# Performance work log

Measured on AMD Instinct MI355X. Metric: run time of the kernel, lower is better.

The kernel has to match this reference:

```python
import jax, jax.numpy as jnp
import numpy as np

N = 100000

def _gcn_layer(x, W, b, src, dst, norm):
    # dense transform then sparse normalized aggregation (scatter-add)
    h = x @ W                                  # [N, out]
    msg = h[src] * norm[:, None]               # [E+N, out]
    agg = jax.ops.segment_sum(msg, dst, num_segments=N)
    return agg + b


def setup_inputs() -> dict:
    key = jax.random.key(0)
    ks = jax.random.split(key, 12)
    num_features, hidden, num_classes = 128, 128, 32
    E = 3200000
    x = jax.random.normal(ks[0], (N, num_features), dtype=jnp.float32)
    edge_index = jax.random.randint(ks[1], (2, E), 0, N, dtype=jnp.int64)

    def glorot(k, fan_in, fan_out):
        s = (6.0 / (fan_in + fan_out)) ** 0.5
        return jax.random.uniform(k, (fan_in, fan_out), jnp.float32, -s, s)

    return {
        "x": x,
        "edge_index": edge_index,
        "W1": glorot(ks[2], num_features, hidden), "b1": jnp.zeros((hidden,), jnp.float32),
        "W2": glorot(ks[3], hidden, hidden),       "b2": jnp.zeros((hidden,), jnp.float32),
        "W3": glorot(ks[4], hidden, hidden),       "b3": jnp.zeros((hidden,), jnp.float32),
        "W4": glorot(ks[5], hidden, num_classes),  "b4": jnp.zeros((num_classes,), jnp.float32),
    }


def reference(x, edge_index, W1, b1, W2, b2, W3, b3, W4, b4):
    # GCNConv semantics: add self-loops, symmetric degree normalization
    loop = jnp.arange(N, dtype=edge_index.dtype)
    src = jnp.concatenate([edge_index[0], loop])   # [E+N]
    dst = jnp.concatenate([edge_index[1], loop])   # [E+N]
    deg = jax.ops.segment_sum(jnp.ones_like(dst, dtype=x.dtype), dst, num_segments=N)
    dinv = jnp.where(deg > 0, deg ** -0.5, 0.0)
    norm = dinv[src] * dinv[dst]                   # [E+N]

    h = _gcn_layer(x, W1, b1, src, dst, norm)
    h = jax.nn.relu(h)                              # dropout: eval mode -> identity
    h = _gcn_layer(h, W2, b2, src, dst, norm)
    h = jax.nn.relu(h)
    h = _gcn_layer(h, W3, b3, src, dst, norm)
    h = jax.nn.relu(h)
    h = _gcn_layer(h, W4, b4, src, dst, norm)
    return jax.nn.log_softmax(h, axis=1)
```

## Files before the change

kernel.cpp:

```cpp
#include <hip/hip_runtime.h>
#include <hip/hip_bf16.h>
#include <math.h>

#define NNODES 100000
#define NBMAX 512
#define CH 8192

typedef __hip_bfloat16 bf16;
typedef __attribute__((ext_vector_type(8))) short short8;
typedef __attribute__((ext_vector_type(4))) float f32x4;
typedef __attribute__((ext_vector_type(2))) float f32x2;

__device__ inline unsigned pack_bf16x2(float a, float b) {
    __hip_bfloat162 p;
    p.x = __float2bfloat16(a);
    p.y = __float2bfloat16(b);
    return *(unsigned*)&p;
}

__device__ inline float2 unpack_bf16x2(unsigned u) {
    __hip_bfloat162 p = *(__hip_bfloat162*)&u;
    return make_float2(__bfloat162float(p.x), __bfloat162float(p.y));
}

__device__ inline unsigned char f32_to_fp8(float v) {
    int p = __builtin_amdgcn_cvt_pk_fp8_f32(v, v, 0, false);
    return (unsigned char)(p & 0xff);
}

__global__ __launch_bounds__(256) void bucket_hist(const int* __restrict__ dst,
                                                   int* __restrict__ bcount, int E, int nb) {
    __shared__ int hist[NBMAX];
    int t = threadIdx.x;
    for (int i = t; i < NBMAX; i += 256) hist[i] = 0;
    __syncthreads();
    int e0 = blockIdx.x * CH;
#pragma unroll
    for (int k = 0; k < 32; ++k) {
        int e = e0 + t + k * 256;
        if (e < E) atomicAdd(&hist[dst[e] >> 8], 1);
    }
    __syncthreads();
    for (int i = t; i < nb; i += 256)
        if (hist[i]) atomicAdd(&bcount[i], hist[i]);
}

__global__ __launch_bounds__(512) void bucket_scan(const int* __restrict__ bcount,
                                                   int* __restrict__ boff,
                                                   int* __restrict__ bcursor,
                                                   int* __restrict__ off, int nb, int n) {
    __shared__ int wsum[8];
    int t = threadIdx.x;
    int v = (t < nb) ? bcount[t] : 0;
    int lane = t & 63, wv = t >> 6;
    int incl = v;
#pragma unroll
    for (int d = 1; d < 64; d <<= 1) {
        int x = __shfl_up(incl, d, 64);
        if (lane >= d) incl += x;
    }
    if (lane == 63) wsum[wv] = incl;
    __syncthreads();
    int wo = 0;
    for (int k = 0; k < wv; ++k) wo += wsum[k];
    int excl = wo + incl - v;
    if (t <= nb) {
        boff[t] = excl;
        if (t < nb) bcursor[t] = excl;
    }
    if (t == nb) off[n] = excl;
}

__global__ __launch_bounds__(256) void partition(const int* __restrict__ src,
                                                 const int* __restrict__ dst,
                                                 int* __restrict__ bcursor,
                                                 int2* __restrict__ part, int E, int nb) {
    __shared__ int hist[NBMAX];
    __shared__ int lstart[NBMAX];
    __shared__ int gbase[NBMAX];
    __shared__ int cursor[NBMAX];
    __shared__ int2 sorted[CH];
    int t = threadIdx.x;
    int e0 = blockIdx.x * CH;
    for (int i = t; i < NBMAX; i += 256) hist[i] = 0;
    __syncthreads();
    int mys[32], myd[32];
#pragma unroll
    for (int k = 0; k < 32; ++k) {
        int e = e0 + t + k * 256;
        int s = 0, d = -1;
        if (e < E) { s = src[e]; d = dst[e]; }
        mys[k] = s; myd[k] = d;
        if (d >= 0) atomicAdd(&hist[d >> 8], 1);
    }
    __syncthreads();
    if (t < 64) {
        int base = t * 8;
        int tmp[8];
        int sum = 0;
#pragma unroll
        for (int j = 0; j < 8; ++j) { tmp[j] = hist[base + j]; sum += tmp[j]; }
        int incl = sum;
#pragma unroll
        for (int d = 1; d < 64; d <<= 1) {
            int x = __shfl_up(incl, d, 64);
            if (t >= d) incl += x;
        }
        int excl = incl - sum;
#pragma unroll
        for (int j = 0; j < 8; ++j) {
            lstart[base + j] = excl;
            cursor[base + j] = excl;
            excl += tmp[j];
        }
    }
    __syncthreads();
    for (int i = t; i < nb; i += 256) {
        int c = hist[i];
        gbase[i] = c ? atomicAdd(&bcursor[i], c) : 0;
    }
    __syncthreads();
#pragma unroll
    for (int k = 0; k < 32; ++k) {
        int d = myd[k];
        if (d >= 0) {
            int lpos = atomicAdd(&cursor[d >> 8], 1);
            sorted[lpos] = make_int2(mys[k], d);
        }
    }
    __syncthreads();
    int cnt = min(CH, E - e0);
    for (int i = t; i < cnt; i += 256) {
        int2 rec = sorted[i];
        int b = rec.y >> 8;
        part[gbase[b] + (i - lstart[b])] = rec;
    }
}

__global__ __launch_bounds__(256) void nodes_fill(const int2* __restrict__ part,
                                                  const int* __restrict__ boff,
                                                  float* __restrict__ dinv,
                                                  int* __restrict__ off,
                                                  int* __restrict__ edges, int n) {
    __shared__ int ndeg[256];
    __shared__ int ws2[4];
    __shared__ int offl[256];
    int b = blockIdx.x;
    int t = threadIdx.x;
    ndeg[t] = 0;
    __syncthreads();
    int r0 = boff[b], r1 = boff[b + 1];
    for (int i = r0 + t; i < r1; i += 256)
        atomicAdd(&ndeg[part[i].y & 255], 1);
    __syncthreads();
    int deg = ndeg[t];
    int node = b * 256 + t;
    int lane = t & 63, wv = t >> 6;
    int incl = deg;
#pragma unroll
    for (int d = 1; d < 64; d <<= 1) {
        int x = __shfl_up(incl, d, 64);
        if (lane >= d) incl += x;
    }
    if (lane == 63) ws2[wv] = incl;
    __syncthreads();
    int wo = 0;
    for (int k = 0; k < wv; ++k) wo += ws2[k];
    int node_off = r0 + wo + incl - deg;
    if (node < n) {
        off[node] = node_off;
        dinv[node] = rsqrtf((float)(deg + 1));
    }
    offl[t] = node_off;
    ndeg[t] = 0;
    __syncthreads();
    for (int i = r0 + t; i < r1; i += 256) {
        int2 rec = part[i];
        int dloc = rec.y & 255;
        int lpos = atomicAdd(&ndeg[dloc], 1);
        edges[offl[dloc] + lpos] = rec.x;
    }
}

__global__ void prep_w(const float* __restrict__ W, bf16* __restrict__ WT, int K, int Nout) {
    int idx = blockIdx.x * blockDim.x + threadIdx.x;
    if (idx >= K * Nout) return;
    int nn = idx / K;
    int kk = idx - nn * K;
    WT[idx] = __float2bfloat16(W[kk * Nout + nn]);
}

#define WSTRIDE 136

__global__ __launch_bounds__(256) void gemm128_f32A(const float* __restrict__ A,
                                                    const bf16* __restrict__ WT,
                                                    const float* __restrict__ dinv,
                                                    unsigned char* __restrict__ C, int n) {
    __shared__ bf16 wl[128 * WSTRIDE];
    int t = threadIdx.x;
#pragma unroll
    for (int l = 0; l < 8; ++l) {
        int chunk = t + l * 256;
        int row = chunk >> 4, ch = chunk & 15;
        *(uint4*)&wl[row * WSTRIDE + ch * 8] = *(const uint4*)&WT[row * 128 + ch * 8];
    }
    __syncthreads();
    int wave = t >> 6, lane = t & 63;
    int m = lane & 15, q = lane >> 4;
    int row_base = blockIdx.x * 128 + wave * 32;
    int r0 = min(row_base + m, n - 1);
    int r1 = min(row_base + 16 + m, n - 1);

    f32x4 acc[2][8];
#pragma unroll
    for (int g = 0; g < 2; ++g)
#pragma unroll
        for (int c = 0; c < 8; ++c) acc[g][c] = (f32x4)(0.f);

#pragma unroll
    for (int kt = 0; kt < 4; ++kt) {
        short8 af[2];
#pragma unroll
        for (int g = 0; g < 2; ++g) {
            const float* ap = &A[(size_t)(g ? r1 : r0) * 128 + kt * 32 + q * 8];
            float4 f0 = *(const float4*)ap;
            float4 f1 = *(const float4*)(ap + 4);
            union { uint4 u; short8 s; } cv;
            cv.u.x = pack_bf16x2(f0.x, f0.y);
            cv.u.y = pack_bf16x2(f0.z, f0.w);
            cv.u.z = pack_bf16x2(f1.x, f1.y);
            cv.u.w = pack_bf16x2(f1.z, f1.w);
            af[g] = cv.s;
        }
#pragma unroll
        for (int c = 0; c < 8; ++c) {
            short8 bf = *(const short8*)&wl[(c * 16 + m) * WSTRIDE + kt * 32 + q * 8];
            acc[0][c] = __builtin_amdgcn_mfma_f32_16x16x32_bf16(af[0], bf, acc[0][c], 0, 0, 0);
            acc[1][c] = __builtin_amdgcn_mfma_f32_16x16x32_bf16(af[1], bf, acc[1][c], 0, 0, 0);
        }
    }
    float dv[2][4];
#pragma unroll
    for (int g = 0; g < 2; ++g)
#pragma unroll
        for (int r = 0; r < 4; ++r) {
            int row = row_base + g * 16 + q * 4 + r;
            dv[g][r] = (row < n) ? dinv[row] : 0.f;
        }
#pragma unroll
    for (int g = 0; g < 2; ++g)
#pragma unroll
        for (int c = 0; c < 8; ++c)
#pragma unroll
            for (int r = 0; r < 4; ++r) {
                int row = row_base + g * 16 + q * 4 + r;
                if (row < n) C[(size_t)row * 128 + c * 16 + m] = f32_to_fp8(acc[g][c][r] * dv[g][r]);
            }
}

__global__ __launch_bounds__(256) void gemm128_bf16A(const bf16* __restrict__ A,
                                                     const bf16* __restrict__ WT,
                                                     const float* __restrict__ dinv,
                                                     unsigned char* __restrict__ C, int n) {
    __shared__ bf16 wl[128 * WSTRIDE];
    int t = threadIdx.x;
#pragma unroll
    for (int l = 0; l < 8; ++l) {
        int chunk = t + l * 256;
        int row = chunk >> 4, ch = chunk & 15;
        *(uint4*)&wl[row * WSTRIDE + ch * 8] = *(const uint4*)&WT[row * 128 + ch * 8];
    }
    __syncthreads();
    int wave = t >> 6, lane = t & 63;
    int m = lane & 15, q = lane >> 4;
    int row_base = blockIdx.x * 128 + wave * 32;
    int r0 = min(row_base + m, n - 1);
    int r1 = min(row_base + 16 + m, n - 1);

    f32x4 acc[2][8];
#pragma unroll
    for (int g = 0; g < 2; ++g)
#pragma unroll
        for (int c = 0; c < 8; ++c) acc[g][c] = (f32x4)(0.f);

#pragma unroll
    for (int kt = 0; kt < 4; ++kt) {
        short8 a0 = *(const short8*)&A[(size_t)r0 * 128 + kt * 32 + q * 8];
        short8 a1 = *(const short8*)&A[(size_t)r1 * 128 + kt * 32 + q * 8];
#pragma unroll
        for (int c = 0; c < 8; ++c) {
            short8 bf = *(const short8*)&wl[(c * 16 + m) * WSTRIDE + kt * 32 + q * 8];
            acc[0][c] = __builtin_amdgcn_mfma_f32_16x16x32_bf16(a0, bf, acc[0][c], 0, 0, 0);
            acc[1][c] = __builtin_amdgcn_mfma_f32_16x16x32_bf16(a1, bf, acc[1][c], 0, 0, 0);
        }
    }
    float dv[2][4];
#pragma unroll
    for (int g = 0; g < 2; ++g)
#pragma unroll
        for (int r = 0; r < 4; ++r) {
            int row = row_base + g * 16 + q * 4 + r;
            dv[g][r] = (row < n) ? dinv[row] : 0.f;
        }
#pragma unroll
    for (int g = 0; g < 2; ++g)
#pragma unroll
        for (int c = 0; c < 8; ++c)
#pragma unroll
            for (int r = 0; r < 4; ++r) {
                int row = row_base + g * 16 + q * 4 + r;
                if (row < n) C[(size_t)row * 128 + c * 16 + m] = f32_to_fp8(acc[g][c][r] * dv[g][r]);
            }
}

__global__ __launch_bounds__(256) void gemm32_bf16A(const bf16* __restrict__ A,
                                                    const bf16* __restrict__ WT,
                                                    const float* __restrict__ dinv,
                                                    bf16* __restrict__ C, int n) {
    int wave = threadIdx.x >> 6;
    int lane = threadIdx.x & 63;
    int m = lane & 15;
    int q = lane >> 4;
    int row_base = blockIdx.x * 64 + wave * 16;
    int arow = min(row_base + m, n - 1);

    f32x4 acc[2];
    acc[0] = (f32x4)(0.f);
    acc[1] = (f32x4)(0.f);

#pragma unroll
    for (int kt = 0; kt < 4; ++kt) {
        short8 af = *(const short8*)&A[(size_t)arow * 128 + kt * 32 + q * 8];
#pragma unroll
        for (int c = 0; c < 2; ++c) {
            short8 bf = *(const short8*)&WT[(size_t)(c * 16 + m) * 128 + kt * 32 + q * 8];
            acc[c] = __builtin_amdgcn_mfma_f32_16x16x32_bf16(af, bf, acc[c], 0, 0, 0);
        }
    }
    float dv[4];
#pragma unroll
    for (int r = 0; r < 4; ++r) {
        int row = row_base + q * 4 + r;
        dv[r] = (row < n) ? dinv[row] : 0.f;
    }
#pragma unroll
    for (int c = 0; c < 2; ++c)
#pragma unroll
        for (int r = 0; r < 4; ++r) {
            int row = row_base + q * 4 + r;
            if (row < n) C[(size_t)row * 32 + c * 16 + m] = __float2bfloat16(acc[c][r] * dv[r]);
        }
}

__global__ __launch_bounds__(256) void agg128(const unsigned char* __restrict__ h,
                                              const int* __restrict__ off,
                                              const int* __restrict__ edges,
                                              const float* __restrict__ dinv,
                                              const float* __restrict__ bias,
                                              bf16* __restrict__ out, int n) {
    int wid = (blockIdx.x * blockDim.x + threadIdx.x) >> 6;
    if (wid >= n) return;
    int lane = threadIdx.x & 63;
    int g = lane >> 4;
    int d = lane & 15;
    const char* hb = (const char*)h;
    unsigned doff = (unsigned)(d << 3);

    f32x2 A0 = {0.f, 0.f}, A1 = {0.f, 0.f}, A2 = {0.f, 0.f}, A3 = {0.f, 0.f};
    {
        uint2 su = *(const uint2*)(hb + (((unsigned)wid << 7) | doff));
        if (g) { su.x = 0u; su.y = 0u; }
        A0 += __builtin_amdgcn_cvt_pk_f32_fp8((int)su.x, false);
        A1 += __builtin_amdgcn_cvt_pk_f32_fp8((int)su.x, true);
        A2 += __builtin_amdgcn_cvt_pk_f32_fp8((int)su.y, false);
        A3 += __builtin_amdgcn_cvt_pk_f32_fp8((int)su.y, true);
    }

    int i0 = off[wid], i1 = off[wid + 1];
    int i = i0;
    int id[8];
    if (i + 32 <= i1) {
#pragma unroll
        for (int j = 0; j < 8; ++j) id[j] = edges[i + j * 4 + g];
    }
    while (i + 32 <= i1) {
        uint2 uu[8];
#pragma unroll
        for (int j = 0; j < 8; ++j)
            uu[j] = *(const uint2*)(hb + (((unsigned)id[j] << 7) | doff));
        int inext = i + 32;
        if (inext + 32 <= i1) {
#pragma unroll
            for (int j = 0; j < 8; ++j) id[j] = edges[inext + j * 4 + g];
        }
#pragma unroll
        for (int j = 0; j < 8; ++j) {
            A0 += __builtin_amdgcn_cvt_pk_f32_fp8((int)uu[j].x, false);
            A1 += __builtin_amdgcn_cvt_pk_f32_fp8((int)uu[j].x, true);
            A2 += __builtin_amdgcn_cvt_pk_f32_fp8((int)uu[j].y, false);
            A3 += __builtin_amdgcn_cvt_pk_f32_fp8((int)uu[j].y, true);
        }
        i = inext;
    }
    if (i < i1) {
        int nj = (i1 - i + 3) >> 2;
        uint2 uu[8];
#pragma unroll
        for (int j = 0; j < 8; ++j) {
            if (j < nj) {
                int e = i + j * 4 + g;
                int s = edges[e];
                if (e >= i1) s = n;
                uu[j] = *(const uint2*)(hb + (((unsigned)s << 7) | doff));
            }
        }
#pragma unroll
        for (int j = 0; j < 8; ++j) {
            if (j < nj) {
                A0 += __builtin_amdgcn_cvt_pk_f32_fp8((int)uu[j].x, false);
                A1 += __builtin_amdgcn_cvt_pk_f32_fp8((int)uu[j].x, true);
                A2 += __builtin_amdgcn_cvt_pk_f32_fp8((int)uu[j].y, false);
                A3 += __builtin_amdgcn_cvt_pk_f32_fp8((int)uu[j].y, true);
            }
        }
    }
    float r0 = A0[0], r1 = A0[1], r2 = A1[0], r3 = A1[1];
    float r4 = A2[0], r5 = A2[1], r6 = A3[0], r7 = A3[1];
    r0 += __shfl_xor(r0, 16); r1 += __shfl_xor(r1, 16);
    r2 += __shfl_xor(r2, 16); r3 += __shfl_xor(r3, 16);
    r4 += __shfl_xor(r4, 16); r5 += __shfl_xor(r5, 16);
    r6 += __shfl_xor(r6, 16); r7 += __shfl_xor(r7, 16);
    r0 += __shfl_xor(r0, 32); r1 += __shfl_xor(r1, 32);
    r2 += __shfl_xor(r2, 32); r3 += __shfl_xor(r3, 32);
    r4 += __shfl_xor(r4, 32); r5 += __shfl_xor(r5, 32);
    r6 += __shfl_xor(r6, 32); r7 += __shfl_xor(r7, 32);
    float pa = (g & 1) ? r2 : r0;
    float pb = (g & 1) ? r3 : r1;
    float qa = (g & 1) ? r6 : r4;
    float qb = (g & 1) ? r7 : r5;
    pa = (g & 2) ? qa : pa;
    pb = (g & 2) ? qb : pb;

    float dl = dinv[wid];
    int od = d * 4 + g;
    float2 bv = *(const float2*)&bias[od * 2];
    float a0 = fmaxf(pa * dl + bv.x, 0.f);
    float a1 = fmaxf(pb * dl + bv.y, 0.f);
    ((unsigned*)out)[(size_t)wid * 64 + od] = pack_bf16x2(a0, a1);
}

__global__ __launch_bounds__(256) void agg32_lsm(const bf16* __restrict__ h,
                                                 const int* __restrict__ off,
                                                 const int* __restrict__ edges,
                                                 const float* __restrict__ dinv,
                                                 const float* __restrict__ bias,
                                                 float* __restrict__ out, int n) {
    int idx = blockIdx.x * blockDim.x + threadIdx.x;
    int node = idx >> 5;
    if (node >= n) return;
    int lane5 = idx & 31;
    int sub = lane5 & 15;
    int pr = lane5 >> 4;
    const unsigned* h4 = (const unsigned*)h;

    unsigned su = pr ? 0u : h4[(size_t)node * 16 + sub];
    float2 sf = unpack_bf16x2(su);
    f32x2 acc = {sf.x, sf.y};

    int i0 = off[node], i1 = off[node + 1];
    int i = i0;
    for (; i + 16 <= i1; i += 16) {
        unsigned uu[8];
#pragma unroll
        for (int j = 0; j < 8; ++j) {
            int s = edges[i + j * 2 + pr];
            uu[j] = h4[(size_t)s * 16 + sub];
        }
#pragma unroll
        for (int j = 0; j < 8; ++j) {
            float2 f = unpack_bf16x2(uu[j]);
            acc[0] += f.x; acc[1] += f.y;
        }
    }
    for (; i + 2 <= i1; i += 2) {
        int s = edges[i + pr];
        float2 f = unpack_bf16x2(h4[(size_t)s * 16 + sub]);
        acc[0] += f.x; acc[1] += f.y;
    }
    if (i < i1) {
        unsigned u = pr ? 0u : h4[(size_t)edges[i] * 16 + sub];
        float2 f = unpack_bf16x2(u);
        acc[0] += f.x; acc[1] += f.y;
    }
    float s0 = acc[0] + __shfl_xor(acc[0], 16);
    float s1 = acc[1] + __shfl_xor(acc[1], 16);

    float dl = dinv[node];
    float2 bv = *(const float2*)&bias[sub * 2];
    float a0 = s0 * dl + bv.x;
    float a1 = s1 * dl + bv.y;
    float m = fmaxf(a0, a1);
    for (int d = 8; d; d >>= 1) m = fmaxf(m, __shfl_xor(m, d));
    float e = expf(a0 - m) + expf(a1 - m);
    for (int d = 8; d; d >>= 1) e += __shfl_xor(e, d);
    float lse = m + logf(e);
    if (pr == 0)
        *(float2*)&out[(size_t)node * 32 + sub * 2] = make_float2(a0 - lse, a1 - lse);
}

extern "C" void kernel_launch(void* const* d_in, const int* in_sizes, int n_in,
                              void* d_out, int out_size, void* d_ws, size_t ws_size,
                              hipStream_t stream) {
    const float* x  = (const float*)d_in[0];
    const int*   ei = (const int*)d_in[1];
    const float* W1 = (const float*)d_in[2];
    const float* b1 = (const float*)d_in[3];
    const float* W2 = (const float*)d_in[4];
    const float* b2 = (const float*)d_in[5];
    const float* W3 = (const float*)d_in[6];
    const float* b3 = (const float*)d_in[7];
    const float* W4 = (const float*)d_in[8];
    const float* b4 = (const float*)d_in[9];
    float* out = (float*)d_out;

    const int N = NNODES;
    const int E = in_sizes[1] / 2;
    const int nb = (N + 255) / 256;

    char* ws = (char*)d_ws;
    size_t o = 0;
    auto alloc = [&](size_t bytes) -> void* {
        void* p = ws + o;
        o += (bytes + 255) & ~(size_t)255;
        return p;
    };
    int*   bcount  = (int*)alloc((size_t)NBMAX * 4);
    int*   boff    = (int*)alloc((size_t)(NBMAX + 1) * 4);
    int*   bcursor = (int*)alloc((size_t)NBMAX * 4);
    int*   off     = (int*)alloc((size_t)(N + 1) * 4);
    float* dinv    = (float*)alloc((size_t)N * 4);
    int2*  part    = (int2*)alloc((size_t)E * 8);
    int*   edges   = (int*)alloc((size_t)(E + 64) * 4);
    bf16*  wt1     = (bf16*)alloc((size_t)128 * 128 * 2);
    bf16*  wt2     = (bf16*)alloc((size_t)128 * 128 * 2);
    bf16*  wt3     = (bf16*)alloc((size_t)128 * 128 * 2);
    bf16*  wt4     = (bf16*)alloc((size_t)32 * 128 * 2);
    unsigned char* hbuf = (unsigned char*)alloc((size_t)(N + 1) * 128);
    bf16*  gbuf    = (bf16*)part;

    const int* srcv = ei;
    const int* dstv = ei + E;

    hipMemsetAsync(bcount, 0, (size_t)NBMAX * 4, stream);
    hipMemsetAsync(hbuf + (size_t)N * 128, 0, 128, stream);

    int pblocks = (E + CH - 1) / CH;
    bucket_hist<<<pblocks, 256, 0, stream>>>(dstv, bcount, E, nb);
    bucket_scan<<<1, 512, 0, stream>>>(bcount, boff, bcursor, off, nb, N);
    partition<<<pblocks, 256, 0, stream>>>(srcv, dstv, bcursor, part, E, nb);
    nodes_fill<<<nb, 256, 0, stream>>>(part, boff, dinv, off, edges, N);

    prep_w<<<64, 256, 0, stream>>>(W1, wt1, 128, 128);
    prep_w<<<64, 256, 0, stream>>>(W2, wt2, 128, 128);
    prep_w<<<64, 256, 0, stream>>>(W3, wt3, 128, 128);
    prep_w<<<16, 256, 0, stream>>>(W4, wt4, 128, 32);

    int gemm128_blocks = (N + 127) / 128;
    int gemm32_blocks = (N + 63) / 64;
    int agg128_blocks = (N + 3) / 4;
    int agg32_blocks = (N * 32 + 255) / 256;

    gemm128_f32A<<<gemm128_blocks, 256, 0, stream>>>(x, wt1, dinv, hbuf, N);
    agg128<<<agg128_blocks, 256, 0, stream>>>(hbuf, off, edges, dinv, b1, gbuf, N);
    gemm128_bf16A<<<gemm128_blocks, 256, 0, stream>>>(gbuf, wt2, dinv, hbuf, N);
    agg128<<<agg128_blocks, 256, 0, stream>>>(hbuf, off, edges, dinv, b2, gbuf, N);
    gemm128_bf16A<<<gemm128_blocks, 256, 0, stream>>>(gbuf, wt3, dinv, hbuf, N);
    agg128<<<agg128_blocks, 256, 0, stream>>>(hbuf, off, edges, dinv, b3, gbuf, N);
    gemm32_bf16A<<<gemm32_blocks, 256, 0, stream>>>(gbuf, wt4, dinv, (bf16*)hbuf, N);
    agg32_lsm<<<agg32_blocks, 256, 0, stream>>>((const bf16*)hbuf, off, edges, dinv, b4, out, N);
}
```

Baseline: 499.2 us.

## Merge setup launches and widen gather batches in aggregation kernels

Folds the four weight-transpose launches and the memsets into a single prep kernel, and fuses the bucket histogram with its scan using a last-block ticket counter. This removes several small launches and memset calls. The 128-wide aggregation now loads 16 indices at a time and gathers without cross-iteration prefetch, and the 32-wide aggregation with log-softmax is restructured so each lane handles 8 bytes per edge over 4 edge groups. The 32-wide path now writes a zero padding row for tail loads. The trade-offs are higher register pressure and a last-block scan that relies on atomics and fences.

```diff
diff --git a/kernel.cpp b/kernel.cpp
--- a/kernel.cpp
+++ b/kernel.cpp
@@ -28,9 +28,41 @@
     return (unsigned char)(p & 0xff);
 }
 
-__global__ __launch_bounds__(256) void bucket_hist(const int* __restrict__ dst,
-                                                   int* __restrict__ bcount, int E, int nb) {
+__global__ __launch_bounds__(256) void prep_w_all(const float* __restrict__ W1, bf16* __restrict__ wt1,
+                                                  const float* __restrict__ W2, bf16* __restrict__ wt2,
+                                                  const float* __restrict__ W3, bf16* __restrict__ wt3,
+                                                  const float* __restrict__ W4, bf16* __restrict__ wt4,
+                                                  int* __restrict__ bcount, int* __restrict__ done,
+                                                  unsigned* __restrict__ zrow) {
+    int b = blockIdx.x, t = threadIdx.x;
+    if (b == 0) {
+        for (int i = t; i < NBMAX; i += 256) bcount[i] = 0;
+        if (t == 0) *done = 0;
+        if (t < 32) zrow[t] = 0u;
+    }
+    const float* W; bf16* WT; int Nout, idx0;
+    if (b < 64)       { W = W1; WT = wt1; Nout = 128; idx0 = b * 256; }
+    else if (b < 128) { W = W2; WT = wt2; Nout = 128; idx0 = (b - 64) * 256; }
+    else if (b < 192) { W = W3; WT = wt3; Nout = 128; idx0 = (b - 128) * 256; }
+    else              { W = W4; WT = wt4; Nout = 32;  idx0 = (b - 192) * 256; }
+    int idx = idx0 + t;
+    if (idx < 128 * Nout) {
+        int nn = idx >> 7;
+        int kk = idx & 127;
+        WT[idx] = __float2bfloat16(W[kk * Nout + nn]);
+    }
+}
+
+__global__ __launch_bounds__(256) void bucket_hist_scan(const int* __restrict__ dst,
+                                                        int* __restrict__ bcount,
+                                                        int* __restrict__ boff,
+                                                        int* __restrict__ bcursor,
+                                                        int* __restrict__ off,
+                                                        int* __restrict__ done,
+                                                        int E, int nb, int n, int nblocks) {
     __shared__ int hist[NBMAX];
+    __shared__ int ticket_s;
+    __shared__ int wsum[4];
     int t = threadIdx.x;
     for (int i = t; i < NBMAX; i += 256) hist[i] = 0;
     __syncthreads();
@@ -43,32 +75,31 @@
     __syncthreads();
     for (int i = t; i < nb; i += 256)
         if (hist[i]) atomicAdd(&bcount[i], hist[i]);
-}
-
-__global__ __launch_bounds__(512) void bucket_scan(const int* __restrict__ bcount,
-                                                   int* __restrict__ boff,
-                                                   int* __restrict__ bcursor,
-                                                   int* __restrict__ off, int nb, int n) {
-    __shared__ int wsum[8];
-    int t = threadIdx.x;
-    int v = (t < nb) ? bcount[t] : 0;
+    __threadfence();
+    __syncthreads();
+    if (t == 0) ticket_s = atomicAdd(done, 1);
+    __syncthreads();
+    if (ticket_s != nblocks - 1) return;
+    __threadfence();
+    int i0 = t * 2, i1v = t * 2 + 1;
+    int a  = (i0  < nb) ? atomicAdd(&bcount[i0], 0) : 0;
+    int bb = (i1v < nb) ? atomicAdd(&bcount[i1v], 0) : 0;
+    int v = a + bb;
     int lane = t & 63, wv = t >> 6;
     int incl = v;
 #pragma unroll
-    for (int d = 1; d < 64; d <<= 1) {
-        int x = __shfl_up(incl, d, 64);
-        if (lane >= d) incl += x;
+    for (int dd = 1; dd < 64; dd <<= 1) {
+        int x = __shfl_up(incl, dd, 64);
+        if (lane >= dd) incl += x;
     }
     if (lane == 63) wsum[wv] = incl;
     __syncthreads();
     int wo = 0;
     for (int k = 0; k < wv; ++k) wo += wsum[k];
     int excl = wo + incl - v;
-    if (t <= nb) {
-        boff[t] = excl;
-        if (t < nb) bcursor[t] = excl;
-    }
-    if (t == nb) off[n] = excl;
+    if (i0 <= nb)  { boff[i0]  = excl;     if (i0  < nb) bcursor[i0]  = excl; }
+    if (i1v <= nb) { boff[i1v] = excl + a; if (i1v < nb) bcursor[i1v] = excl + a; }
+    if (t == 255) off[n] = excl + v;
 }
 
 __global__ __launch_bounds__(256) void partition(const int* __restrict__ src,
@@ -182,14 +213,6 @@
     }
 }
 
-__global__ void prep_w(const float* __restrict__ W, bf16* __restrict__ WT, int K, int Nout) {
-    int idx = blockIdx.x * blockDim.x + threadIdx.x;
-    if (idx >= K * Nout) return;
-    int nn = idx / K;
-    int kk = idx - nn * K;
-    WT[idx] = __float2bfloat16(W[kk * Nout + nn]);
-}
-
 #define WSTRIDE 136
 
 __global__ __launch_bounds__(256) void gemm128_f32A(const float* __restrict__ A,
@@ -317,6 +340,8 @@
                                                     const bf16* __restrict__ WT,
                                                     const float* __restrict__ dinv,
                                                     bf16* __restrict__ C, int n) {
+    if (blockIdx.x == 0 && threadIdx.x < 32)
+        C[(size_t)n * 32 + threadIdx.x] = __float2bfloat16(0.f);
     int wave = threadIdx.x >> 6;
     int lane = threadIdx.x & 63;
     int m = lane & 15;
@@ -378,44 +403,42 @@
 
     int i0 = off[wid], i1 = off[wid + 1];
     int i = i0;
-    int id[8];
-    if (i + 32 <= i1) {
-#pragma unroll
-        for (int j = 0; j < 8; ++j) id[j] = edges[i + j * 4 + g];
-    }
-    while (i + 32 <= i1) {
-        uint2 uu[8];
-#pragma unroll
-        for (int j = 0; j < 8; ++j)
-            uu[j] = *(const uint2*)(hb + (((unsigned)id[j] << 7) | doff));
-        int inext = i + 32;
-        if (inext + 32 <= i1) {
-#pragma unroll
-            for (int j = 0; j < 8; ++j) id[j] = edges[inext + j * 4 + g];
-        }
-#pragma unroll
-        for (int j = 0; j < 8; ++j) {
+    while (i1 - i > 64) {
+        int id2[16];
+#pragma unroll
+        for (int j = 0; j < 16; ++j) id2[j] = edges[i + j * 4 + g];
+        uint2 uu[16];
+#pragma unroll
+        for (int j = 0; j < 16; ++j)
+            uu[j] = *(const uint2*)(hb + (((unsigned)id2[j] << 7) | doff));
+#pragma unroll
+        for (int j = 0; j < 16; ++j) {
             A0 += __builtin_amdgcn_cvt_pk_f32_fp8((int)uu[j].x, false);
             A1 += __builtin_amdgcn_cvt_pk_f32_fp8((int)uu[j].x, true);
             A2 += __builtin_amdgcn_cvt_pk_f32_fp8((int)uu[j].y, false);
             A3 += __builtin_amdgcn_cvt_pk_f32_fp8((int)uu[j].y, true);
         }
-        i = inext;
-    }
-    if (i < i1) {
-        int nj = (i1 - i + 3) >> 2;
-        uint2 uu[8];
-#pragma unroll
-        for (int j = 0; j < 8; ++j) {
+        i += 64;
+    }
+    {
+        int rem = i1 - i;
+        int nj = (rem + 3) >> 2;
+        int id2[16];
+        uint2 uu[16];
+#pragma unroll
+        for (int j = 0; j < 16; ++j) {
             if (j < nj) {
                 int e = i + j * 4 + g;
                 int s = edges[e];
                 if (e >= i1) s = n;
-                uu[j] = *(const uint2*)(hb + (((unsigned)s << 7) | doff));
+                id2[j] = s;
             }
         }
 #pragma unroll
-        for (int j = 0; j < 8; ++j) {
+        for (int j = 0; j < 16; ++j)
+            if (j < nj) uu[j] = *(const uint2*)(hb + (((unsigned)id2[j] << 7) | doff));
+#pragma unroll
+        for (int j = 0; j < 16; ++j) {
             if (j < nj) {
                 A0 += __builtin_amdgcn_cvt_pk_f32_fp8((int)uu[j].x, false);
                 A1 += __builtin_amdgcn_cvt_pk_f32_fp8((int)uu[j].x, true);
@@ -459,53 +482,80 @@
     int node = idx >> 5;
     if (node >= n) return;
     int lane5 = idx & 31;
-    int sub = lane5 & 15;
-    int pr = lane5 >> 4;
-    const unsigned* h4 = (const unsigned*)h;
-
-    unsigned su = pr ? 0u : h4[(size_t)node * 16 + sub];
-    float2 sf = unpack_bf16x2(su);
-    f32x2 acc = {sf.x, sf.y};
-
+    int g = lane5 >> 3;
+    int d = lane5 & 7;
+    const char* hb = (const char*)h;
+    unsigned doff = (unsigned)(d << 3);
+
+    f32x2 acc0 = {0.f, 0.f}, acc1 = {0.f, 0.f};
+    {
+        uint2 su = *(const uint2*)(hb + (((unsigned)node << 6) | doff));
+        if (g) { su.x = 0u; su.y = 0u; }
+        float2 f0 = unpack_bf16x2(su.x), f1 = unpack_bf16x2(su.y);
+        acc0[0] += f0.x; acc0[1] += f0.y; acc1[0] += f1.x; acc1[1] += f1.y;
+    }
     int i0 = off[node], i1 = off[node + 1];
     int i = i0;
-    for (; i + 16 <= i1; i += 16) {
-        unsigned uu[8];
-#pragma unroll
-        for (int j = 0; j < 8; ++j) {
-            int s = edges[i + j * 2 + pr];
-            uu[j] = h4[(size_t)s * 16 + sub];
-        }
-#pragma unroll
-        for (int j = 0; j < 8; ++j) {
-            float2 f = unpack_bf16x2(uu[j]);
-            acc[0] += f.x; acc[1] += f.y;
-        }
-    }
-    for (; i + 2 <= i1; i += 2) {
-        int s = edges[i + pr];
-        float2 f = unpack_bf16x2(h4[(size_t)s * 16 + sub]);
-        acc[0] += f.x; acc[1] += f.y;
-    }
-    if (i < i1) {
-        unsigned u = pr ? 0u : h4[(size_t)edges[i] * 16 + sub];
-        float2 f = unpack_bf16x2(u);
-        acc[0] += f.x; acc[1] += f.y;
-    }
-    float s0 = acc[0] + __shfl_xor(acc[0], 16);
-    float s1 = acc[1] + __shfl_xor(acc[1], 16);
+    while (i1 - i > 64) {
+        int id2[16];
+#pragma unroll
+        for (int j = 0; j < 16; ++j) id2[j] = edges[i + j * 4 + g];
+        uint2 uu[16];
+#pragma unroll
+        for (int j = 0; j < 16; ++j)
+            uu[j] = *(const uint2*)(hb + (((unsigned)id2[j] << 6) | doff));
+#pragma unroll
+        for (int j = 0; j < 16; ++j) {
+            float2 f0 = unpack_bf16x2(uu[j].x), f1 = unpack_bf16x2(uu[j].y);
+            acc0[0] += f0.x; acc0[1] += f0.y; acc1[0] += f1.x; acc1[1] += f1.y;
+        }
+        i += 64;
+    }
+    {
+        int rem = i1 - i;
+        int nj = (rem + 3) >> 2;
+        int id2[16];
+        uint2 uu[16];
+#pragma unroll
+        for (int j = 0; j < 16; ++j) {
+            if (j < nj) {
+                int e = i + j * 4 + g;
+                int s = edges[e];
+                if (e >= i1) s = n;
+                id2[j] = s;
+            }
+        }
+#pragma unroll
+        for (int j = 0; j < 16; ++j)
+            if (j < nj) uu[j] = *(const uint2*)(hb + (((unsigned)id2[j] << 6) | doff));
+#pragma unroll
+        for (int j = 0; j < 16; ++j) {
+            if (j < nj) {
+                float2 f0 = unpack_bf16x2(uu[j].x), f1 = unpack_bf16x2(uu[j].y);
+                acc0[0] += f0.x; acc0[1] += f0.y; acc1[0] += f1.x; acc1[1] += f1.y;
+            }
+        }
+    }
+    float s0 = acc0[0], s1 = acc0[1], s2 = acc1[0], s3 = acc1[1];
+    s0 += __shfl_xor(s0, 8);  s1 += __shfl_xor(s1, 8);
+    s2 += __shfl_xor(s2, 8);  s3 += __shfl_xor(s3, 8);
+    s0 += __shfl_xor(s0, 16); s1 += __shfl_xor(s1, 16);
+    s2 += __shfl_xor(s2, 16); s3 += __shfl_xor(s3, 16);
 
     float dl = dinv[node];
-    float2 bv = *(const float2*)&bias[sub * 2];
+    float4 bv = *(const float4*)&bias[d * 4];
     float a0 = s0 * dl + bv.x;
     float a1 = s1 * dl + bv.y;
-    float m = fmaxf(a0, a1);
-    for (int d = 8; d; d >>= 1) m = fmaxf(m, __shfl_xor(m, d));
-    float e = expf(a0 - m) + expf(a1 - m);
-    for (int d = 8; d; d >>= 1) e += __shfl_xor(e, d);
+    float a2 = s2 * dl + bv.z;
+    float a3 = s3 * dl + bv.w;
+    float m = fmaxf(fmaxf(a0, a1), fmaxf(a2, a3));
+    for (int dd = 1; dd < 8; dd <<= 1) m = fmaxf(m, __shfl_xor(m, dd));
+    float e = expf(a0 - m) + expf(a1 - m) + expf(a2 - m) + expf(a3 - m);
+    for (int dd = 1; dd < 8; dd <<= 1) e += __shfl_xor(e, dd);
     float lse = m + logf(e);
-    if (pr == 0)
-        *(float2*)&out[(size_t)node * 32 + sub * 2] = make_float2(a0 - lse, a1 - lse);
+    if (g == 0)
+        *(float4*)&out[(size_t)node * 32 + d * 4] =
+            make_float4(a0 - lse, a1 - lse, a2 - lse, a3 - lse);
 }
 
 extern "C" void kernel_launch(void* const* d_in, const int* in_sizes, int n_in,
@@ -537,6 +587,7 @@
     int*   bcount  = (int*)alloc((size_t)NBMAX * 4);
     int*   boff    = (int*)alloc((size_t)(NBMAX + 1) * 4);
     int*   bcursor = (int*)alloc((size_t)NBMAX * 4);
+    int*   done    = (int*)alloc(4);
     int*   off     = (int*)alloc((size_t)(N + 1) * 4);
     float* dinv    = (float*)alloc((size_t)N * 4);
     int2*  part    = (int2*)alloc((size_t)E * 8);
@@ -551,19 +602,14 @@
     const int* srcv = ei;
     const int* dstv = ei + E;
 
-    hipMemsetAsync(bcount, 0, (size_t)NBMAX * 4, stream);
-    hipMemsetAsync(hbuf + (size_t)N * 128, 0, 128, stream);
-
     int pblocks = (E + CH - 1) / CH;
-    bucket_hist<<<pblocks, 256, 0, stream>>>(dstv, bcount, E, nb);
-    bucket_scan<<<1, 512, 0, stream>>>(bcount, boff, bcursor, off, nb, N);
+
+    prep_w_all<<<208, 256, 0, stream>>>(W1, wt1, W2, wt2, W3, wt3, W4, wt4,
+                                        bcount, done, (unsigned*)(hbuf + (size_t)N * 128));
+    bucket_hist_scan<<<pblocks, 256, 0, stream>>>(dstv, bcount, boff, bcursor, off, done,
+                                                  E, nb, N, pblocks);
     partition<<<pblocks, 256, 0, stream>>>(srcv, dstv, bcursor, part, E, nb);
     nodes_fill<<<nb, 256, 0, stream>>>(part, boff, dinv, off, edges, N);
-
-    prep_w<<<64, 256, 0, stream>>>(W1, wt1, 128, 128);
-    prep_w<<<64, 256, 0, stream>>>(W2, wt2, 128, 128);
-    prep_w<<<64, 256, 0, stream>>>(W3, wt3, 128, 128);
-    prep_w<<<16, 256, 0, stream>>>(W4, wt4, 128, 32);
 
     int gemm128_blocks = (N + 127) / 128;
     int gemm32_blocks = (N + 63) / 64;
```

After: 536.4 us. 7.5% more time.
